# Optimization experiments

Hardware: AMD Instinct MI355X
Metric: run time of the kernel (lower is better)

## Reference

```python
import jax, jax.numpy as jnp
import numpy as np

B, C, H, W = 1024, 3, 32, 32
NCLS = 10

def _conv(x, w, b, padding):
    y = jax.lax.conv_general_dilated(x, w, (1, 1), padding, dimension_numbers=('NCHW', 'OIHW', 'NCHW'))
    return y + b[None, :, None, None]

def _maxpool2(x):
    return jax.lax.reduce_window(x, -jnp.inf, jax.lax.max, (1, 1, 2, 2), (1, 1, 2, 2), 'VALID')

def _lenet(x, lw1, lb1, lw2, lb2, lfc1, lfb1, lfc2, lfb2, lfc3, lfb3):
    h = jax.nn.relu(_conv(x, lw1, lb1, 'VALID'))   # [B,6,28,28]
    h = _maxpool2(h)                               # [B,6,14,14]
    h = jax.nn.relu(_conv(h, lw2, lb2, 'VALID'))   # [B,16,10,10]
    h = _maxpool2(h)                               # [B,16,5,5]
    h = h.reshape(h.shape[0], -1)                  # [B,400]
    h = jax.nn.relu(h @ lfc1 + lfb1)
    h = jax.nn.relu(h @ lfc2 + lfb2)
    return h @ lfc3 + lfb3                         # [B,10]

def _resnet(x, rw0, rb0, rw1a, rb1a, rw1b, rb1b, rw2a, rb2a, rw2b, rb2b, rfc, rfb):
    h = jax.nn.relu(_conv(x, rw0, rb0, 'SAME'))    # [B,64,32,32]
    r = jax.nn.relu(_conv(h, rw1a, rb1a, 'SAME'))
    r = _conv(r, rw1b, rb1b, 'SAME')
    h = jax.nn.relu(h + r)
    r = jax.nn.relu(_conv(h, rw2a, rb2a, 'SAME'))
    r = _conv(r, rw2b, rb2b, 'SAME')
    h = jax.nn.relu(h + r)
    h = h.mean(axis=(2, 3))                        # [B,64]
    return h @ rfc + rfb                           # [B,10]

def setup_inputs():
    key = jax.random.key(0)
    ks = jax.random.split(key, 16)
    def w(k, shape, fan_in):
        return jax.random.normal(k, shape, jnp.float32) * np.float32(1.0 / np.sqrt(fan_in))
    return {
        'x': jax.random.normal(ks[0], (B, C, H, W), jnp.float32),
        'threshold': jnp.float32(0.3),
        'labels': jax.random.randint(ks[1], (B,), 0, NCLS),
        'lw1': w(ks[2], (6, 3, 5, 5), 75), 'lb1': jnp.zeros((6,), jnp.float32),
        'lw2': w(ks[3], (16, 6, 5, 5), 150), 'lb2': jnp.zeros((16,), jnp.float32),
        'lfc1': w(ks[4], (400, 120), 400), 'lfb1': jnp.zeros((120,), jnp.float32),
        'lfc2': w(ks[5], (120, 84), 120), 'lfb2': jnp.zeros((84,), jnp.float32),
        'lfc3': w(ks[6], (84, NCLS), 84), 'lfb3': jnp.zeros((NCLS,), jnp.float32),
        'rw0': w(ks[7], (64, 3, 3, 3), 27), 'rb0': jnp.zeros((64,), jnp.float32),
        'rw1a': w(ks[8], (64, 64, 3, 3), 576), 'rb1a': jnp.zeros((64,), jnp.float32),
        'rw1b': w(ks[9], (64, 64, 3, 3), 576), 'rb1b': jnp.zeros((64,), jnp.float32),
        'rw2a': w(ks[10], (64, 64, 3, 3), 576), 'rb2a': jnp.zeros((64,), jnp.float32),
        'rw2b': w(ks[11], (64, 64, 3, 3), 576), 'rb2b': jnp.zeros((64,), jnp.float32),
        'rfc': w(ks[12], (64, NCLS), 64), 'rfb': jnp.zeros((NCLS,), jnp.float32),
    }

def reference(x, threshold, labels, lw1, lb1, lw2, lb2, lfc1, lfb1, lfc2, lfb2, lfc3, lfb3, rw0, rb0, rw1a, rb1a, rw1b, rb1b, rw2a, rb2a, rw2b, rb2b, rfc, rfb):
    out = _lenet(x, lw1, lb1, lw2, lb2, lfc1, lfb1, lfc2, lfb2, lfc3, lfb3)
    pred = jnp.argmax(out, axis=1)
    # fused confusion-matrix update: single scatter-add replaces the 10x10 python loop
    conf_matrix = jnp.zeros((NCLS, NCLS), jnp.float32).at[labels, pred].add(1.0)
    probs = jax.nn.softmax(out, axis=1)
    top2, _ = jax.lax.top_k(probs, 2)
    low_conf = (top2[:, 0] - top2[:, 1]) <= threshold    # [B] bool
    # batched fallback: one grouped resnet call + masked merge replaces the per-sample loop
    res_out = _resnet(x, rw0, rb0, rw1a, rb1a, rw1b, rb1b, rw2a, rb2a, rw2b, rb2b, rfc, rfb)
    out = jnp.where(low_conf[:, None], res_out, out)
    return out, conf_matrix
```

## Files before the change

kernel.cpp:

```cpp
#include <hip/hip_runtime.h>
#include <hip/hip_bf16.h>
#include <math.h>

#define BATCH 1024

typedef __attribute__((ext_vector_type(8))) short bf16x8;
typedef __attribute__((ext_vector_type(4))) float f32x4;

#define IMG_ELEMS 73984
#define IMG_B 147968
#define ROW_B 4352
#define CH_B 544
#define WT_OFF 43520
#define WT_HALF_B 36864

__global__ __launch_bounds__(256) void lenet_conv1(const float* __restrict__ x,
    const float* __restrict__ w, const float* __restrict__ bias, float* __restrict__ p1)
{
    __shared__ float img[3 * 1024];
    __shared__ float wl[450];
    __shared__ float bl[6];
    int b = blockIdx.x, t = threadIdx.x;
    for (int i = t; i < 3072; i += 256) img[i] = x[(size_t)b * 3072 + i];
    for (int i = t; i < 450; i += 256) wl[i] = w[i];
    if (t < 6) bl[t] = bias[t];
    __syncthreads();
    for (int idx = t; idx < 1176; idx += 256) {
        int o = idx / 196, r = idx - o * 196, py = r / 14, px = r - py * 14;
        int y0 = 2 * py, x0 = 2 * px;
        float s00, s01, s10, s11;
        s00 = s01 = s10 = s11 = bl[o];
        for (int c = 0; c < 3; c++) {
            float pv[6][6];
            #pragma unroll
            for (int i2 = 0; i2 < 6; i2++)
                #pragma unroll
                for (int j2 = 0; j2 < 6; j2++)
                    pv[i2][j2] = img[c * 1024 + (y0 + i2) * 32 + x0 + j2];
            const float* wc = &wl[o * 75 + c * 25];
            #pragma unroll
            for (int ky = 0; ky < 5; ky++)
                #pragma unroll
                for (int kx = 0; kx < 5; kx++) {
                    float wv = wc[ky * 5 + kx];
                    s00 += pv[ky][kx] * wv;
                    s01 += pv[ky][kx + 1] * wv;
                    s10 += pv[ky + 1][kx] * wv;
                    s11 += pv[ky + 1][kx + 1] * wv;
                }
        }
        float m = fmaxf(fmaxf(s00, s01), fmaxf(s10, s11));
        p1[(size_t)b * 1176 + idx] = fmaxf(m, 0.f);
    }
}

__global__ __launch_bounds__(256) void lenet_conv2(const float* __restrict__ p1,
    const float* __restrict__ w, const float* __restrict__ bias, float* __restrict__ p2)
{
    __shared__ float img[1176];
    __shared__ float wl[2400];
    __shared__ float bl[16];
    int b = blockIdx.x, t = threadIdx.x;
    for (int i = t; i < 1176; i += 256) img[i] = p1[(size_t)b * 1176 + i];
    for (int i = t; i < 2400; i += 256) wl[i] = w[i];
    if (t < 16) bl[t] = bias[t];
    __syncthreads();
    for (int idx = t; idx < 400; idx += 256) {
        int o = idx / 25, r = idx - o * 25, py = r / 5, px = r - py * 5;
        int y0 = 2 * py, x0 = 2 * px;
        float s00, s01, s10, s11;
        s00 = s01 = s10 = s11 = bl[o];
        for (int c = 0; c < 6; c++) {
            float pv[6][6];
            #pragma unroll
            for (int i2 = 0; i2 < 6; i2++)
                #pragma unroll
                for (int j2 = 0; j2 < 6; j2++)
                    pv[i2][j2] = img[c * 196 + (y0 + i2) * 14 + x0 + j2];
            const float* wc = &wl[o * 150 + c * 25];
            #pragma unroll
            for (int ky = 0; ky < 5; ky++)
                #pragma unroll
                for (int kx = 0; kx < 5; kx++) {
                    float wv = wc[ky * 5 + kx];
                    s00 += pv[ky][kx] * wv;
                    s01 += pv[ky][kx + 1] * wv;
                    s10 += pv[ky + 1][kx] * wv;
                    s11 += pv[ky + 1][kx + 1] * wv;
                }
        }
        float m = fmaxf(fmaxf(s00, s01), fmaxf(s10, s11));
        p2[(size_t)b * 400 + idx] = fmaxf(m, 0.f);
    }
}

__global__ __launch_bounds__(256) void lenet_fc(const float* __restrict__ p2,
    const float* __restrict__ w1, const float* __restrict__ b1,
    const float* __restrict__ w2, const float* __restrict__ b2,
    const float* __restrict__ w3, const float* __restrict__ b3,
    const int* __restrict__ labels, const float* __restrict__ thr,
    float* __restrict__ out, float* __restrict__ conf, int* __restrict__ flags)
{
    __shared__ float xin[400];
    __shared__ float h1[120];
    __shared__ float h2[84];
    __shared__ float ps[256];
    __shared__ float lg[10];
    int b = blockIdx.x, t = threadIdx.x;
    for (int i = t; i < 400; i += 256) xin[i] = p2[(size_t)b * 400 + i];
    __syncthreads();
    {
        int n = t & 127, half = t >> 7;
        float s = 0.f;
        if (n < 120) {
            int k0 = half * 200;
            for (int k = k0; k < k0 + 200; k++) s += xin[k] * w1[k * 120 + n];
        }
        ps[t] = s;
    }
    __syncthreads();
    if (t < 120) h1[t] = fmaxf(ps[t] + ps[t + 128] + b1[t], 0.f);
    __syncthreads();
    {
        int n = t & 127, half = t >> 7;
        float s = 0.f;
        if (n < 84) {
            int k0 = half * 60;
            for (int k = k0; k < k0 + 60; k++) s += h1[k] * w2[k * 84 + n];
        }
        ps[t] = s;
    }
    __syncthreads();
    if (t < 84) h2[t] = fmaxf(ps[t] + ps[t + 128] + b2[t], 0.f);
    __syncthreads();
    if (t < 10) {
        float s = b3[t];
        for (int k = 0; k < 84; k++) s += h2[k] * w3[k * 10 + t];
        lg[t] = s;
        out[(size_t)b * 10 + t] = s;
    }
    __syncthreads();
    if (t == 0) {
        int pred = 0;
        float m = lg[0];
        #pragma unroll
        for (int j = 1; j < 10; j++) if (lg[j] > m) { m = lg[j]; pred = j; }
        float se = 0.f, m2 = -1e30f;
        #pragma unroll
        for (int j = 0; j < 10; j++) {
            se += expf(lg[j] - m);
            if (j != pred) m2 = fmaxf(m2, lg[j]);
        }
        float gap = (1.f - expf(m2 - m)) / se;
        flags[b] = (gap <= thr[0]) ? 1 : 0;
        atomicAdd(&conf[labels[b] * 10 + pred], 1.f);
    }
}

__global__ __launch_bounds__(256) void prep_weights(
    const float* __restrict__ w0, const float* __restrict__ w1,
    const float* __restrict__ w2, const float* __restrict__ w3,
    __hip_bfloat16* __restrict__ dst)
{
    int tid = blockIdx.x * 256 + threadIdx.x;
    if (tid >= 4 * 36864) return;
    int c = tid / 36864, r = tid - c * 36864;
    int tap = r / 4096, r2 = r - tap * 4096;
    int co = r2 >> 6, ci = r2 & 63;
    const float* src = (c == 0) ? w0 : (c == 1) ? w1 : (c == 2) ? w2 : w3;
    float v = src[((size_t)co * 64 + ci) * 9 + tap];
    int nh = co >> 5, nt = (co >> 4) & 1, m = co & 15;
    int kb = ci >> 5, q = (ci >> 3) & 3, e = ci & 7;
    size_t elem = (size_t)(c * 2 + nh) * 18432
                + (size_t)((tap * 2 + kb) * 2 + nt) * 512 + q * 128 + m * 8 + e;
    dst[elem] = __float2bfloat16(v);
}

__global__ __launch_bounds__(256) void prep_w0t(const float* __restrict__ w,
                                                float* __restrict__ dst)
{
    int tid = blockIdx.x * 256 + threadIdx.x;
    if (tid >= 1728) return;
    int k = tid >> 6, co = tid & 63;
    dst[tid] = w[co * 27 + k];
}

__global__ __launch_bounds__(256) void zero_borders(__hip_bfloat16* __restrict__ buf, int cb)
{
    int tid = blockIdx.x * 256 + threadIdx.x;
    int total = cb * 132 * 8;
    if (tid >= total) return;
    int img = tid / 1056, r = tid - img * 1056;
    int pxi = r >> 3, chunk = r & 7;
    int row, col;
    if (pxi < 34)       { row = 0;  col = pxi; }
    else if (pxi < 68)  { row = 33; col = pxi - 34; }
    else if (pxi < 100) { row = pxi - 67; col = 0; }
    else                { row = pxi - 99; col = 33; }
    uint4 z = {0, 0, 0, 0};
    *(uint4*)((char*)buf + (size_t)img * IMG_B + (size_t)row * ROW_B
              + chunk * CH_B + col * 16) = z;
}

__global__ __launch_bounds__(256) void conv0_nhwc(const float* __restrict__ x,
    const float* __restrict__ wT, const float* __restrict__ bias,
    __hip_bfloat16* __restrict__ out, int cb)
{
    __shared__ char smem[8 * ROW_B];
    float* sl = (float*)smem;
    int bid = blockIdx.x;
    int img = bid % cb, strip = bid / cb;
    int r0 = strip * 8;
    int t = threadIdx.x;
    const float* xi = x + (size_t)img * 3072;
    for (int i = t; i < 1020; i += 256) {
        int c = i / 340, rr2 = i - c * 340;
        int rr = rr2 / 34, cc = rr2 - rr * 34;
        int y = r0 + rr - 1, xx = cc - 1;
        float v = 0.f;
        if (y >= 0 && y < 32 && xx >= 0 && xx < 32) v = xi[c * 1024 + y * 32 + xx];
        sl[(c * 10 + rr) * 34 + cc] = v;
    }
    __syncthreads();

    int rr = t >> 5, col = t & 31;
    float iv[27];
    #pragma unroll
    for (int c = 0; c < 3; c++)
        #pragma unroll
        for (int dy = 0; dy < 3; dy++)
            #pragma unroll
            for (int dx = 0; dx < 3; dx++)
                iv[c * 9 + dy * 3 + dx] = sl[(c * 10 + rr + dy) * 34 + col + dx];
    __syncthreads();

    float s[64];
    #pragma unroll
    for (int co = 0; co < 64; co++) s[co] = bias[co];
    #pragma unroll
    for (int k = 0; k < 27; k++) {
        const float v = iv[k];
        const float* wk = wT + k * 64;
        #pragma unroll
        for (int co = 0; co < 64; co++) s[co] = fmaf(v, wk[co], s[co]);
    }
    __hip_bfloat16 ov[64];
    #pragma unroll
    for (int co = 0; co < 64; co++) ov[co] = __float2bfloat16(fmaxf(s[co], 0.f));

    char* brow = smem + rr * ROW_B + (col + 1) * 16;
    const uint4* srcv = (const uint4*)ov;
    #pragma unroll
    for (int j = 0; j < 8; j++) *(uint4*)(brow + j * CH_B) = srcv[j];
    if (t < 128) {
        int row = t >> 4, ch = (t >> 1) & 7, side = t & 1;
        uint4 z = {0, 0, 0, 0};
        *(uint4*)(smem + row * ROW_B + ch * CH_B + (side ? 33 : 0) * 16) = z;
    }
    __syncthreads();
    char* gbase = (char*)out + (size_t)img * IMG_B + (size_t)(r0 + 1) * ROW_B;
    for (int u = t; u < 2176; u += 256)
        *(uint4*)(gbase + (size_t)u * 16) = *(const uint4*)(smem + (size_t)u * 16);
}

#define GLL(gp, lp)                                                            \
    __builtin_amdgcn_global_load_lds(                                          \
        (const __attribute__((address_space(1))) unsigned int*)(gp),           \
        (__attribute__((address_space(3))) unsigned int*)(lp), 16, 0, 0)

template<bool ADD>
__global__ __launch_bounds__(256, 1) void conv3x3_lds(
    const __hip_bfloat16* __restrict__ act, const __hip_bfloat16* __restrict__ wts,
    const float* __restrict__ bias, const __hip_bfloat16* __restrict__ skip,
    __hip_bfloat16* __restrict__ out, int cb)
{
    __shared__ char sl[WT_OFF + 2 * WT_HALF_B];
    int img = blockIdx.x;
    int t = threadIdx.x;
    int w = t >> 6, lane = t & 63;
    int m = lane & 15, q = lane >> 4;

    const char* gimg = (const char*)act + (size_t)img * IMG_B;

    const char* gw = (const char*)wts;
    for (int u0 = w * 64; u0 < 4608; u0 += 256)
        GLL(gw + (size_t)(u0 + lane) * 16, sl + WT_OFF + u0 * 16);
    for (int u0 = w * 64; u0 < 2720; u0 += 256) {
        int u = u0 + lane;
        if (u < 2720) GLL(gimg + (size_t)u * 16, sl + u0 * 16);
    }
    __syncthreads();

    int abase[4];
    #pragma unroll
    for (int mt = 0; mt < 4; mt++)
        abase[mt] = (2 * w + (mt >> 1)) * ROW_B + ((mt & 1) * 16 + m) * 16 + q * CH_B;
    int bbase[4];
    #pragma unroll
    for (int nt = 0; nt < 4; nt++)
        bbase[nt] = WT_OFF + (nt >> 1) * WT_HALF_B + (nt & 1) * 1024 + q * 256 + m * 16;
    float bv[4];
    #pragma unroll
    for (int nt = 0; nt < 4; nt++) bv[nt] = bias[nt * 16 + m];

    for (int strip = 0; strip < 4; ++strip) {
        f32x4 acc[4][4] = {};
        bf16x8 a[2][4], b[2][4];

        #define ALOAD(s, buf)                                                  \
            {                                                                  \
                const int tap_ = (s) >> 1, kb_ = (s) & 1;                      \
                const int dy_ = tap_ / 3, dx_ = tap_ - dy_ * 3;                \
                const int aoff_ = dy_ * ROW_B + kb_ * (4 * CH_B) + dx_ * 16;   \
                _Pragma("unroll")                                              \
                for (int mt = 0; mt < 4; mt++)                                 \
                    a[buf][mt] = *(const bf16x8*)(sl + abase[mt] + aoff_);     \
            }
        #define BLOAD(s, buf)                                                  \
            {                                                                  \
                const int boff_ = ((s) >> 1) * 4096 + ((s) & 1) * 2048;        \
                _Pragma("unroll")                                              \
                for (int nt = 0; nt < 4; nt++)                                 \
                    b[buf][nt] = *(const bf16x8*)(sl + bbase[nt] + boff_);     \
            }

        ALOAD(0, 0) BLOAD(0, 0)
        #pragma unroll
        for (int s = 0; s < 18; s++) {
            int cur = s & 1;
            if (s < 17) { ALOAD(s + 1, cur ^ 1) BLOAD(s + 1, cur ^ 1) }
            #pragma unroll
            for (int mt = 0; mt < 4; mt++)
                #pragma unroll
                for (int nt = 0; nt < 4; nt++)
                    acc[mt][nt] = __builtin_amdgcn_mfma_f32_16x16x32_bf16(
                        a[cur][mt], b[cur][nt], acc[mt][nt], 0, 0, 0);
        }
        #undef ALOAD
        #undef BLOAD

        __syncthreads();

        #pragma unroll
        for (int nt = 0; nt < 4; nt++) {
            #pragma unroll
            for (int mt = 0; mt < 4; mt++) {
                int pl = (2 * w + (mt >> 1)) * 32 + (mt & 1) * 16 + q * 4;
                #pragma unroll
                for (int r = 0; r < 4; r++) {
                    __hip_bfloat16 hv = __float2bfloat16(acc[mt][nt][r] + bv[nt]);
                    *(__hip_bfloat16*)(sl + (size_t)(pl + r) * 136
                                       + (nt * 16 + m) * 2) = hv;
                }
            }
        }
        __syncthreads();

        {
            char* oimg = (char*)out + (size_t)img * IMG_B;
            const char* simg = (const char*)skip + (size_t)img * IMG_B;
            int ch = t >> 5, px = t & 31;
            #pragma unroll
            for (int pass = 0; pass < 8; pass++) {
                size_t goff = (size_t)(strip * 8 + 1 + pass) * ROW_B
                            + ch * CH_B + (px + 1) * 16;
                bf16x8 v = *(const bf16x8*)(sl + (size_t)(pass * 32 + px) * 136 + ch * 16);
                bf16x8 o;
                if (ADD) {
                    bf16x8 sv = *(const bf16x8*)(simg + goff);
                    #pragma unroll
                    for (int e = 0; e < 8; e++) {
                        float f = __bfloat162float(((__hip_bfloat16*)&v)[e])
                                + __bfloat162float(((__hip_bfloat16*)&sv)[e]);
                        ((__hip_bfloat16*)&o)[e] = __float2bfloat16(fmaxf(f, 0.f));
                    }
                } else {
                    #pragma unroll
                    for (int e = 0; e < 8; e++) {
                        float f = __bfloat162float(((__hip_bfloat16*)&v)[e]);
                        ((__hip_bfloat16*)&o)[e] = __float2bfloat16(fmaxf(f, 0.f));
                    }
                }
                *(bf16x8*)(oimg + goff) = o;
            }
        }

        if (strip < 3) {
            __syncthreads();
            const char* gn = gimg + (size_t)(strip + 1) * (8 * ROW_B);
            for (int u0 = w * 64; u0 < 2720; u0 += 256) {
                int u = u0 + lane;
                if (u < 2720) GLL(gn + (size_t)u * 16, sl + u0 * 16);
            }
            __syncthreads();
        }
    }
}

__global__ __launch_bounds__(256) void res_head_bf16(const __hip_bfloat16* __restrict__ h,
    const float* __restrict__ rfc, const float* __restrict__ rfb,
    const int* __restrict__ flags, float* __restrict__ out)
{
    __shared__ float part[4][64];
    __shared__ float mns[64];
    int img = blockIdx.x, t = threadIdx.x;
    int w = t >> 6, lane = t & 63;
    int c = lane & 7;
    const char* base = (const char*)h + (size_t)img * IMG_B;

    float s8[8];
    #pragma unroll
    for (int j = 0; j < 8; j++) s8[j] = 0.f;

    for (int ry = 0; ry < 8; ry++) {
        int row = w * 8 + ry + 1;
        const char* rb = base + (size_t)row * ROW_B;
        #pragma unroll
        for (int k = 0; k < 4; k++) {
            int g = lane + 64 * k;
            bf16x8 v = *(const bf16x8*)(rb + c * CH_B + ((g >> 3) + 1) * 16);
            #pragma unroll
            for (int j = 0; j < 8; j++)
                s8[j] += __bfloat162float(*(__hip_bfloat16*)&((short*)&v)[j]);
        }
    }
    #pragma unroll
    for (int off = 8; off <= 32; off <<= 1)
        #pragma unroll
        for (int j = 0; j < 8; j++) s8[j] += __shfl_xor(s8[j], off, 64);
    if (lane < 8)
        #pragma unroll
        for (int j = 0; j < 8; j++) part[w][c * 8 + j] = s8[j];
    __syncthreads();
    if (t < 64) mns[t] = (part[0][t] + part[1][t] + part[2][t] + part[3][t]) * (1.f / 1024.f);
    __syncthreads();
    if (t < 10 && flags[img]) {
        float s2 = rfb[t];
        for (int cc = 0; cc < 64; cc++) s2 += mns[cc] * rfc[cc * 10 + t];
        out[(size_t)img * 10 + t] = s2;
    }
}

extern "C" void kernel_launch(void* const* d_in, const int* in_sizes, int n_in,
                              void* d_out, int out_size, void* d_ws, size_t ws_size,
                              hipStream_t stream)
{
    const float* x    = (const float*)d_in[0];
    const float* thr  = (const float*)d_in[1];
    const int*   labels = (const int*)d_in[2];
    const float* lw1 = (const float*)d_in[3];  const float* lb1 = (const float*)d_in[4];
    const float* lw2 = (const float*)d_in[5];  const float* lb2 = (const float*)d_in[6];
    const float* lfc1 = (const float*)d_in[7]; const float* lfb1 = (const float*)d_in[8];
    const float* lfc2 = (const float*)d_in[9]; const float* lfb2 = (const float*)d_in[10];
    const float* lfc3 = (const float*)d_in[11];const float* lfb3 = (const float*)d_in[12];
    const float* rw0 = (const float*)d_in[13]; const float* rb0 = (const float*)d_in[14];
    const float* rw1a = (const float*)d_in[15];const float* rb1a = (const float*)d_in[16];
    const float* rw1b = (const float*)d_in[17];const float* rb1b = (const float*)d_in[18];
    const float* rw2a = (const float*)d_in[19];const float* rb2a = (const float*)d_in[20];
    const float* rw2b = (const float*)d_in[21];const float* rb2b = (const float*)d_in[22];
    const float* rfc = (const float*)d_in[23]; const float* rfb = (const float*)d_in[24];

    float* out  = (float*)d_out;
    float* conf = out + (size_t)BATCH * 10;

    int nc = 1;
    while (nc < 16 &&
           2ull * (size_t)(BATCH / nc) * 147968ull + 294912ull + 16384ull > ws_size)
        nc <<= 1;
    int cb = BATCH / nc;

    __hip_bfloat16* A  = (__hip_bfloat16*)d_ws;
    __hip_bfloat16* Bb = A + (size_t)cb * IMG_ELEMS;
    __hip_bfloat16* wprep = Bb + (size_t)cb * IMG_ELEMS;
    int* flags = (int*)((char*)wprep + 294912);
    float* w0t = (float*)((char*)wprep + 294912 + 4096);

    float* p1 = (float*)A;
    float* p2 = p1 + 1204224;

    hipMemsetAsync(conf, 0, 100 * sizeof(float), stream);

    prep_weights<<<(4 * 36864 + 255) / 256, 256, 0, stream>>>(rw1a, rw1b, rw2a, rw2b, wprep);
    prep_w0t<<<7, 256, 0, stream>>>(rw0, w0t);

    lenet_conv1<<<BATCH, 256, 0, stream>>>(x, lw1, lb1, p1);
    lenet_conv2<<<BATCH, 256, 0, stream>>>(p1, lw2, lb2, p2);
    lenet_fc<<<BATCH, 256, 0, stream>>>(p2, lfc1, lfb1, lfc2, lfb2, lfc3, lfb3,
                                        labels, thr, out, conf, flags);

    int zb = (cb * 1056 + 255) / 256;
    zero_borders<<<zb, 256, 0, stream>>>(A, cb);
    zero_borders<<<zb, 256, 0, stream>>>(Bb, cb);

    const __hip_bfloat16* W1a = wprep;
    const __hip_bfloat16* W1b = wprep + 36864;
    const __hip_bfloat16* W2a = wprep + 2 * 36864;
    const __hip_bfloat16* W2b = wprep + 3 * 36864;

    for (int c0 = 0; c0 < BATCH; c0 += cb) {
        const float* xc = x + (size_t)c0 * 3072;
        conv0_nhwc<<<cb * 4, 256, 0, stream>>>(xc, w0t, rb0, A, cb);
        conv3x3_lds<false><<<cb, 256, 0, stream>>>(A,  W1a, rb1a, nullptr, Bb, cb);
        conv3x3_lds<true ><<<cb, 256, 0, stream>>>(Bb, W1b, rb1b, A, A, cb);
        conv3x3_lds<false><<<cb, 256, 0, stream>>>(A,  W2a, rb2a, nullptr, Bb, cb);
        conv3x3_lds<true ><<<cb, 256, 0, stream>>>(Bb, W2b, rb2b, A, A, cb);
        res_head_bf16<<<cb, 256, 0, stream>>>(A, rfc, rfb, flags + c0, out + (size_t)c0 * 10);
    }
}
```

Measured before the change: 726.2 us.

## Double-buffer activation strips in LDS to overlap loads with MFMA compute

Splits the LDS activation area in conv3x3_lds into two buffers and issues the global_load_lds for the next strip before the current strip's MFMA loop, so the load latency overlaps with compute. Weights move to offset zero, and the __syncthreads calls become explicit s_waitcnt plus s_barrier pairs. This grows LDS use to about 157 KB per block. It also makes correctness depend on the hand-written waitcnt ordering: the epilogue stores to the current buffer while loads into the other buffer are still in flight.

Result: no change. 730.1 us (+0.5%).

```diff
diff --git a/kernel.cpp b/kernel.cpp
--- a/kernel.cpp
+++ b/kernel.cpp
@@ -11,8 +11,9 @@
 #define IMG_B 147968
 #define ROW_B 4352
 #define CH_B 544
-#define WT_OFF 43520
 #define WT_HALF_B 36864
+#define ACT_A_OFF 73728
+#define ACT_B_OFF 117248
 
 __global__ __launch_bounds__(256) void lenet_conv1(const float* __restrict__ x,
     const float* __restrict__ w, const float* __restrict__ bias, float* __restrict__ p1)
@@ -274,7 +275,7 @@
     const float* __restrict__ bias, const __hip_bfloat16* __restrict__ skip,
     __hip_bfloat16* __restrict__ out, int cb)
 {
-    __shared__ char sl[WT_OFF + 2 * WT_HALF_B];
+    __shared__ char sl[160768];
     int img = blockIdx.x;
     int t = threadIdx.x;
     int w = t >> 6, lane = t & 63;
@@ -284,12 +285,13 @@
 
     const char* gw = (const char*)wts;
     for (int u0 = w * 64; u0 < 4608; u0 += 256)
-        GLL(gw + (size_t)(u0 + lane) * 16, sl + WT_OFF + u0 * 16);
+        GLL(gw + (size_t)(u0 + lane) * 16, sl + u0 * 16);
     for (int u0 = w * 64; u0 < 2720; u0 += 256) {
         int u = u0 + lane;
-        if (u < 2720) GLL(gimg + (size_t)u * 16, sl + u0 * 16);
-    }
-    __syncthreads();
+        if (u < 2720) GLL(gimg + (size_t)u * 16, sl + ACT_A_OFF + u0 * 16);
+    }
+    asm volatile("s_waitcnt vmcnt(0)" ::: "memory");
+    asm volatile("s_barrier" ::: "memory");
 
     int abase[4];
     #pragma unroll
@@ -298,14 +300,26 @@
     int bbase[4];
     #pragma unroll
     for (int nt = 0; nt < 4; nt++)
-        bbase[nt] = WT_OFF + (nt >> 1) * WT_HALF_B + (nt & 1) * 1024 + q * 256 + m * 16;
+        bbase[nt] = (nt >> 1) * WT_HALF_B + (nt & 1) * 1024 + q * 256 + m * 16;
     float bv[4];
     #pragma unroll
     for (int nt = 0; nt < 4; nt++) bv[nt] = bias[nt * 16 + m];
 
+    int curo = ACT_A_OFF;
     for (int strip = 0; strip < 4; ++strip) {
+        int nxto = (ACT_A_OFF + ACT_B_OFF) - curo;
+
+        if (strip < 3) {
+            const char* gn = gimg + (size_t)(strip + 1) * (8 * ROW_B);
+            for (int u0 = w * 64; u0 < 2720; u0 += 256) {
+                int u = u0 + lane;
+                if (u < 2720) GLL(gn + (size_t)u * 16, sl + nxto + u0 * 16);
+            }
+        }
+
         f32x4 acc[4][4] = {};
         bf16x8 a[2][4], b[2][4];
+        const char* ab = sl + curo;
 
         #define ALOAD(s, buf)                                                  \
             {                                                                  \
@@ -314,7 +328,7 @@
                 const int aoff_ = dy_ * ROW_B + kb_ * (4 * CH_B) + dx_ * 16;   \
                 _Pragma("unroll")                                              \
                 for (int mt = 0; mt < 4; mt++)                                 \
-                    a[buf][mt] = *(const bf16x8*)(sl + abase[mt] + aoff_);     \
+                    a[buf][mt] = *(const bf16x8*)(ab + abase[mt] + aoff_);     \
             }
         #define BLOAD(s, buf)                                                  \
             {                                                                  \
@@ -339,7 +353,8 @@
         #undef ALOAD
         #undef BLOAD
 
-        __syncthreads();
+        asm volatile("s_waitcnt lgkmcnt(0)" ::: "memory");
+        asm volatile("s_barrier" ::: "memory");
 
         #pragma unroll
         for (int nt = 0; nt < 4; nt++) {
@@ -349,12 +364,13 @@
                 #pragma unroll
                 for (int r = 0; r < 4; r++) {
                     __hip_bfloat16 hv = __float2bfloat16(acc[mt][nt][r] + bv[nt]);
-                    *(__hip_bfloat16*)(sl + (size_t)(pl + r) * 136
+                    *(__hip_bfloat16*)(sl + curo + (size_t)(pl + r) * 136
                                        + (nt * 16 + m) * 2) = hv;
                 }
             }
         }
-        __syncthreads();
+        asm volatile("s_waitcnt lgkmcnt(0)" ::: "memory");
+        asm volatile("s_barrier" ::: "memory");
 
         {
             char* oimg = (char*)out + (size_t)img * IMG_B;
@@ -364,7 +380,8 @@
             for (int pass = 0; pass < 8; pass++) {
                 size_t goff = (size_t)(strip * 8 + 1 + pass) * ROW_B
                             + ch * CH_B + (px + 1) * 16;
-                bf16x8 v = *(const bf16x8*)(sl + (size_t)(pass * 32 + px) * 136 + ch * 16);
+                bf16x8 v = *(const bf16x8*)(sl + curo
+                            + (size_t)(pass * 32 + px) * 136 + ch * 16);
                 bf16x8 o;
                 if (ADD) {
                     bf16x8 sv = *(const bf16x8*)(simg + goff);
@@ -385,15 +402,10 @@
             }
         }
 
-        if (strip < 3) {
-            __syncthreads();
-            const char* gn = gimg + (size_t)(strip + 1) * (8 * ROW_B);
-            for (int u0 = w * 64; u0 < 2720; u0 += 256) {
-                int u = u0 + lane;
-                if (u < 2720) GLL(gn + (size_t)u * 16, sl + u0 * 16);
-            }
-            __syncthreads();
-        }
+        asm volatile("s_waitcnt lgkmcnt(0)" ::: "memory");
+        if (strip < 3) asm volatile("s_waitcnt vmcnt(0)" ::: "memory");
+        asm volatile("s_barrier" ::: "memory");
+        curo = nxto;
     }
 }
 
```
